# Performance work log

Measured on AMD Instinct MI355X. Metric: run time of the kernel, lower is better.

Reference implementation:

```python
import jax, jax.numpy as jnp
import numpy as np

NUM_CLASSES = 64  # matches labels fill_max
EMB_SCALE = 0.1   # keeps pairwise distances small so exp() stays finite (same regime as trained embeddings)


def setup_inputs() -> dict:
    key = jax.random.key(0)
    k1, k2 = jax.random.split(key)
    embeddings = jax.random.normal(k1, (8192, 128), dtype=jnp.float32) * EMB_SCALE
    labels = jax.random.randint(k2, (8192,), 0, NUM_CLASSES, dtype=jnp.int64 if jax.config.jax_enable_x64 else jnp.int32)
    return {"embeddings": embeddings, "labels": labels}


def reference(embeddings, labels):
    # Squared-euclidean distance matrix: ||xi||^2 + ||xj||^2 - 2 xi.xj   [N,N]
    sq = jnp.sum(embeddings * embeddings, axis=1)
    D = sq[:, None] + sq[None, :] - 2.0 * (embeddings @ embeddings.T)

    N = embeddings.shape[0]
    same = labels[:, None] == labels[None, :]          # [N,N] same-label mask
    neg = jnp.logical_not(same)

    # Z_i = sum over negatives n of exp(D[i,n]); then for pair (i,j):
    # sum_n exp(D[i,n] - D[i,j]) = Z_i * exp(-D[i,j])  (exact same math, factored)
    Z = jnp.sum(jnp.where(neg, jnp.exp(D), 0.0), axis=1)  # [N]

    # anchor-positive pairs: combinations(label_indices, 2) => i<j, same label
    iu = jnp.arange(N)
    pair_mask = same & (iu[:, None] < iu[None, :])

    # per-pair loss: log(1 + sum_n exp(D[a,n] - D[a,p]))
    L = jnp.log1p(Z[:, None] * jnp.exp(-D))            # [N,N]

    row_sum = jnp.sum(jnp.where(pair_mask, L, 0.0), axis=1)   # anchor i contributes pairs with label labels[i]
    row_cnt = jnp.sum(pair_mask, axis=1).astype(L.dtype)

    label_sum = jax.ops.segment_sum(row_sum, labels, num_segments=NUM_CLASSES)
    label_cnt = jax.ops.segment_sum(row_cnt, labels, num_segments=NUM_CLASSES)

    valid = label_cnt > 0                               # classes with >=2 members
    label_mean = jnp.where(valid, label_sum / jnp.maximum(label_cnt, 1.0), 0.0)
    n_valid = jnp.sum(valid)
    loss = jnp.sum(label_mean) / jnp.maximum(n_valid, 1).astype(L.dtype)
    return loss
```

## Files before the change

### kernel.cpp

```cpp
#include <hip/hip_runtime.h>
#include <hip/hip_bf16.h>
#include <math.h>

#define KD 128
#define NCLS 64
#define LOG2E 1.4426950408889634f
#define NEG2L -2.8853900817779268f
#define POS2L 2.8853900817779268f
#define LN2 0.6931471805599453f

typedef __attribute__((ext_vector_type(8))) short short8;
typedef __attribute__((ext_vector_type(4))) float f32x4;

__device__ inline void gload_lds16(const void* g, void* l) {
    __builtin_amdgcn_global_load_lds((const __attribute__((address_space(1))) unsigned int*)g,
                                     (__attribute__((address_space(3))) unsigned int*)l,
                                     16, 0, 0);
}
__device__ __forceinline__ float vexp2(float x) { float r; asm("v_exp_f32 %0, %1" : "=v"(r) : "v"(x)); return r; }
__device__ __forceinline__ float vlog2(float x) { float r; asm("v_log_f32 %0, %1" : "=v"(r) : "v"(x)); return r; }

__global__ __launch_bounds__(256) void prep_kernel(const float* __restrict__ emb,
                                                   const int* __restrict__ lab,
                                                   short* __restrict__ embb,
                                                   float* __restrict__ s2,
                                                   float* __restrict__ Z,
                                                   float* __restrict__ lsum,
                                                   int* __restrict__ cnt,
                                                   int* __restrict__ off,
                                                   int* __restrict__ list,
                                                   int* __restrict__ ctr, int N) {
    const int tid = threadIdx.x;
    if (blockIdx.x == gridDim.x - 1) {
        __shared__ int cntL[NCLS], offL[NCLS], curL[NCLS];
        if (tid < NCLS) cntL[tid] = 0;
        __syncthreads();
        for (int i = tid; i < N; i += 256) atomicAdd(&cntL[lab[i]], 1);
        __syncthreads();
        if (tid < NCLS) {
            int v = cntL[tid];
            int s = v;
            for (int m = 1; m < 64; m <<= 1) {
                int t2 = __shfl_up(s, m, 64);
                if (tid >= m) s += t2;
            }
            offL[tid] = s - v;
            curL[tid] = 0;
            off[tid] = s - v;
            cnt[tid] = v;
            lsum[tid] = 0.f;
        }
        if (tid == 0) ctr[0] = 0;
        __syncthreads();
        for (int i = tid; i < N; i += 256) {
            int c = lab[i];
            int p = atomicAdd(&curL[c], 1);
            list[offL[c] + p] = i;
        }
    } else {
        const int b = blockIdx.x;
        const int r0 = b * 16;
        const size_t base = (size_t)r0 * KD;
        float4 a = *(const float4*)&emb[base + (size_t)tid * 8];
        float4 bb = *(const float4*)&emb[base + (size_t)tid * 8 + 4];
        short8 o;
        __hip_bfloat16 h;
        h = __float2bfloat16(a.x);  o[0] = *(short*)&h;
        h = __float2bfloat16(a.y);  o[1] = *(short*)&h;
        h = __float2bfloat16(a.z);  o[2] = *(short*)&h;
        h = __float2bfloat16(a.w);  o[3] = *(short*)&h;
        h = __float2bfloat16(bb.x); o[4] = *(short*)&h;
        h = __float2bfloat16(bb.y); o[5] = *(short*)&h;
        h = __float2bfloat16(bb.z); o[6] = *(short*)&h;
        h = __float2bfloat16(bb.w); o[7] = *(short*)&h;
        *(short8*)&embb[base + (size_t)tid * 8] = o;
        float s = a.x * a.x + a.y * a.y + a.z * a.z + a.w * a.w
                + bb.x * bb.x + bb.y * bb.y + bb.z * bb.z + bb.w * bb.w;
        s += __shfl_xor(s, 1, 64);
        s += __shfl_xor(s, 2, 64);
        s += __shfl_xor(s, 4, 64);
        s += __shfl_xor(s, 8, 64);
        if ((tid & 15) == 0) s2[r0 + (tid >> 4)] = s * LOG2E;
        if (tid < 16) Z[r0 + tid] = 0.f;
    }
}

__global__ __launch_bounds__(256, 2) void zmain_kernel(const short* __restrict__ embb,
                                                       const float* __restrict__ s2,
                                                       float* __restrict__ Z, int N) {
    __shared__ short8 As8[128 * 16];
    __shared__ short8 Bs8[128 * 16];

    const int tid = threadIdx.x;
    const int w = tid >> 6, l = tid & 63;
    const int wr = w >> 1, wc = w & 1;
    const int g = blockIdx.x, it = blockIdx.y;
    const int i0 = it * 128;
    const short8* embv = (const short8*)embb;
    const int nd = 4 + ((g == 7 && it < 32) ? 1 : 0);

#pragma unroll
    for (int itr = 0; itr < 8; ++itr) {
        int lr = w * 32 + itr * 4 + (l >> 4);
        int c = (l & 15) ^ (lr & 7);
        gload_lds16(embv + (size_t)(i0 + lr) * 16 + c, &As8[w * 512 + itr * 64]);
    }
    {
        int j0 = ((it + g * 4) & 63) * 128;
#pragma unroll
        for (int itr = 0; itr < 8; ++itr) {
            int lr = w * 32 + itr * 4 + (l >> 4);
            int c = (l & 15) ^ (lr & 7);
            gload_lds16(embv + (size_t)(j0 + lr) * 16 + c, &Bs8[w * 512 + itr * 64]);
        }
    }

    float s2i[4][4];
#pragma unroll
    for (int mi = 0; mi < 4; ++mi)
#pragma unroll
        for (int r = 0; r < 4; ++r)
            s2i[mi][r] = s2[i0 + wr * 64 + mi * 16 + (l >> 4) * 4 + r];
    float zsum[4][4];
#pragma unroll
    for (int mi = 0; mi < 4; ++mi)
#pragma unroll
        for (int r = 0; r < 4; ++r) zsum[mi][r] = 0.f;

    __syncthreads();

    short8 af[4][4];
#pragma unroll
    for (int mi = 0; mi < 4; ++mi) {
        int row = wr * 64 + mi * 16 + (l & 15);
        int rs = row * 16, rx = row & 7;
#pragma unroll
        for (int ks = 0; ks < 4; ++ks) {
            int kc = ks * 4 + (l >> 4);
            af[mi][ks] = As8[rs + (kc ^ rx)];
        }
    }
    __syncthreads();

    for (int t = 0; t < nd; ++t) {
        const int d = (t < 4) ? (g * 4 + t) : 32;
        const int j0 = ((it + d) & 63) * 128;
        short8* rb = (t & 1) ? As8 : Bs8;
        short8* sb = (t & 1) ? Bs8 : As8;
        if (t + 1 < nd) {
            const int d1 = (t + 1 < 4) ? (g * 4 + t + 1) : 32;
            int j1 = ((it + d1) & 63) * 128;
#pragma unroll
            for (int itr = 0; itr < 8; ++itr) {
                int lr = w * 32 + itr * 4 + (l >> 4);
                int c = (l & 15) ^ (lr & 7);
                gload_lds16(embv + (size_t)(j1 + lr) * 16 + c, &sb[w * 512 + itr * 64]);
            }
        }

        f32x4 acc[4][4];
#pragma unroll
        for (int mi = 0; mi < 4; ++mi)
#pragma unroll
            for (int ni = 0; ni < 4; ++ni) acc[mi][ni] = (f32x4){0.f, 0.f, 0.f, 0.f};

#pragma unroll
        for (int ks = 0; ks < 4; ++ks) {
            short8 bf[4];
            int kc = ks * 4 + (l >> 4);
#pragma unroll
            for (int ni = 0; ni < 4; ++ni) {
                int row = wc * 64 + ni * 16 + (l & 15);
                bf[ni] = rb[row * 16 + (kc ^ (row & 7))];
            }
#pragma unroll
            for (int mi = 0; mi < 4; ++mi)
#pragma unroll
                for (int ni = 0; ni < 4; ++ni)
                    acc[mi][ni] = __builtin_amdgcn_mfma_f32_16x16x32_bf16(af[mi][ks], bf[ni], acc[mi][ni], 0, 0, 0);
        }

        float s2j[4];
#pragma unroll
        for (int ni = 0; ni < 4; ++ni)
            s2j[ni] = s2[j0 + wc * 64 + ni * 16 + (l & 15)];
        float cs[4] = {0.f, 0.f, 0.f, 0.f};
#pragma unroll
        for (int mi = 0; mi < 4; ++mi)
#pragma unroll
            for (int ni = 0; ni < 4; ++ni)
#pragma unroll
                for (int r = 0; r < 4; ++r) {
                    float e = vexp2(fmaf(NEG2L, acc[mi][ni][r], s2i[mi][r] + s2j[ni]));
                    zsum[mi][r] += e;
                    cs[ni] += e;
                }
        if (d > 0) {
#pragma unroll
            for (int ni = 0; ni < 4; ++ni) {
                float v = cs[ni];
                v += __shfl_xor(v, 16, 64);
                v += __shfl_xor(v, 32, 64);
                if ((l >> 4) == 0)
                    atomicAdd(&Z[j0 + wc * 64 + ni * 16 + (l & 15)], v);
            }
        }
        __syncthreads();
    }

#pragma unroll
    for (int mi = 0; mi < 4; ++mi)
#pragma unroll
        for (int r = 0; r < 4; ++r) {
            float v = zsum[mi][r];
            v += __shfl_xor(v, 1, 64);
            v += __shfl_xor(v, 2, 64);
            v += __shfl_xor(v, 4, 64);
            v += __shfl_xor(v, 8, 64);
            if ((l & 15) == 0)
                atomicAdd(&Z[i0 + wr * 64 + mi * 16 + (l >> 4) * 4 + r], v);
        }
}

__device__ __forceinline__ void gram_quad(const short8* Ms8, int l, int wr, int wc,
                                          int qi, int qj, f32x4 acc[4][4]) {
#pragma unroll
    for (int mi = 0; mi < 4; ++mi)
#pragma unroll
        for (int ni = 0; ni < 4; ++ni) acc[mi][ni] = (f32x4){0.f, 0.f, 0.f, 0.f};
#pragma unroll
    for (int ks = 0; ks < 4; ++ks) {
        short8 af[4], bf[4];
        int kc = ks * 4 + (l >> 4);
#pragma unroll
        for (int mi = 0; mi < 4; ++mi) {
            int row = qi * 128 + wr * 64 + mi * 16 + (l & 15);
            af[mi] = Ms8[row * 16 + (kc ^ (row & 7))];
        }
#pragma unroll
        for (int ni = 0; ni < 4; ++ni) {
            int row = qj * 128 + wc * 64 + ni * 16 + (l & 15);
            bf[ni] = Ms8[row * 16 + (kc ^ (row & 7))];
        }
#pragma unroll
        for (int mi = 0; mi < 4; ++mi)
#pragma unroll
            for (int ni = 0; ni < 4; ++ni)
                acc[mi][ni] = __builtin_amdgcn_mfma_f32_16x16x32_bf16(af[mi], bf[ni], acc[mi][ni], 0, 0, 0);
    }
}

__global__ __launch_bounds__(256, 2) void loss_kernel(const short* __restrict__ embb,
                                                      const float* __restrict__ s2,
                                                      const float* __restrict__ Z,
                                                      const int* __restrict__ cnt,
                                                      const int* __restrict__ off,
                                                      const int* __restrict__ list,
                                                      float* __restrict__ lsum,
                                                      int* __restrict__ ctr,
                                                      float* __restrict__ out) {
    __shared__ short8 Ms8[256 * 16];
    __shared__ float s2L[256], zfL[256], zsubL[256];
    __shared__ int gidL[256];
    __shared__ float red[4];
    __shared__ int lastB;

    const int h = blockIdx.x, c = blockIdx.y;
    const int k = cnt[c], base = off[c];
    const int kp = min(k, 256);
    const int tid = threadIdx.x;
    const int w = tid >> 6, l = tid & 63;
    const int wr = w >> 1, wc = w & 1;
    const short8* embv = (const short8*)embb;

    const bool active = (k >= 2) && !(h == 1 && kp <= 128);
    if (active) {
        {
            int gg = list[base + min(tid, k - 1)];
            bool ok = tid < k;
            s2L[tid] = ok ? s2[gg] : 0.f;
            gidL[tid] = ok ? gg : 0x7fffffff;
            zsubL[tid] = 0.f;
        }
#pragma unroll
        for (int itr = 0; itr < 16; ++itr) {
            int grp = w * 16 + itr;
            if (grp * 4 >= kp) break;
            int lr = grp * 4 + (l >> 4);
            int ch = (l & 15) ^ (lr & 7);
            int gg = list[base + min(lr, k - 1)];
            gload_lds16(embv + (size_t)gg * 16 + ch, &Ms8[grp * 64]);
        }
        __syncthreads();

        const int two = (kp > 128);
        f32x4 acc[4][4];

        for (int qq = 0; qq <= 2 * two; ++qq) {
            int qi = (qq == 2) ? 1 : 0;
            int qj = (qq == 0) ? 0 : 1;
            gram_quad(Ms8, l, wr, wc, qi, qj, acc);
            float rowsum[4][4];
#pragma unroll
            for (int mi = 0; mi < 4; ++mi)
#pragma unroll
                for (int r = 0; r < 4; ++r) rowsum[mi][r] = 0.f;
            float colsum[4] = {0.f, 0.f, 0.f, 0.f};
#pragma unroll
            for (int mi = 0; mi < 4; ++mi)
#pragma unroll
                for (int ni = 0; ni < 4; ++ni) {
                    int pB = qi * 128 + wr * 64 + mi * 16 + (l >> 4) * 4;
                    int qL = qj * 128 + wc * 64 + ni * 16 + (l & 15);
                    float sj = s2L[qL];
#pragma unroll
                    for (int r = 0; r < 4; ++r) {
                        float e = vexp2(fmaf(NEG2L, acc[mi][ni][r], s2L[pB + r] + sj));
                        e = ((pB + r) < k && qL < k) ? e : 0.f;
                        rowsum[mi][r] += e;
                        colsum[ni] += e;
                    }
                }
#pragma unroll
            for (int mi = 0; mi < 4; ++mi)
#pragma unroll
                for (int r = 0; r < 4; ++r) {
                    float v = rowsum[mi][r];
                    v += __shfl_xor(v, 1, 64);
                    v += __shfl_xor(v, 2, 64);
                    v += __shfl_xor(v, 4, 64);
                    v += __shfl_xor(v, 8, 64);
                    if ((l & 15) == 0)
                        atomicAdd(&zsubL[qi * 128 + wr * 64 + mi * 16 + (l >> 4) * 4 + r], v);
                }
            if (qi != qj) {
#pragma unroll
                for (int ni = 0; ni < 4; ++ni) {
                    float v = colsum[ni];
                    v += __shfl_xor(v, 16, 64);
                    v += __shfl_xor(v, 32, 64);
                    if ((l >> 4) == 0)
                        atomicAdd(&zsubL[qj * 128 + wc * 64 + ni * 16 + (l & 15)], v);
                }
            }
        }
        __syncthreads();
        zfL[tid] = (tid < k) ? (Z[gidL[tid]] - zsubL[tid]) : 0.f;
        __syncthreads();

        float part = 0.f;
        int q0 = (h == 0) ? 0 : 2;
        int q1 = (h == 0) ? (two ? 1 : 0) : 2;
        for (int qq = q0; qq <= q1; ++qq) {
            int qi = (qq == 2) ? 1 : 0;
            int qj = (qq == 0) ? 0 : 1;
            gram_quad(Ms8, l, wr, wc, qi, qj, acc);
#pragma unroll
            for (int mi = 0; mi < 4; ++mi)
#pragma unroll
                for (int ni = 0; ni < 4; ++ni) {
                    int qL = qj * 128 + wc * 64 + ni * 16 + (l & 15);
                    float sj = s2L[qL];
                    float zq = zfL[qL];
                    int gb = gidL[qL];
#pragma unroll
                    for (int r = 0; r < 4; ++r) {
                        int pL = qi * 128 + wr * 64 + mi * 16 + (l >> 4) * 4 + r;
                        bool valid = (pL < qL) && (qL < k);
                        float arg = fmaf(POS2L, acc[mi][ni][r], -(s2L[pL] + sj));
                        arg = valid ? arg : -160.f;
                        float e = vexp2(arg);
                        float z = (gidL[pL] < gb) ? zfL[pL] : zq;
                        part += vlog2(fmaf(z, e, 1.0f));
                    }
                }
        }

        for (int m = 32; m; m >>= 1) part += __shfl_xor(part, m, 64);
        if (l == 0) red[w] = part;
        __syncthreads();
        if (tid == 0)
            atomicAdd(&lsum[c], red[0] + red[1] + red[2] + red[3]);
    }

    __threadfence();
    if (tid == 0) lastB = (atomicAdd(ctr, 1) == 2 * NCLS - 1);
    __syncthreads();
    if (lastB) {
        __threadfence();
        if (tid < 64) {
            int cc = tid;
            float ls = atomicAdd(&lsum[cc], 0.0f);
            int kk = atomicAdd((int*)&cnt[cc], 0);
            float mean = 0.f;
            int valid = 0;
            long np = (long)kk * (kk - 1) / 2;
            if (np > 0) { mean = ls * LN2 / (float)np; valid = 1; }
            for (int m = 32; m; m >>= 1) {
                mean += __shfl_xor(mean, m, 64);
                valid += __shfl_xor(valid, m, 64);
            }
            if (cc == 0) out[0] = mean / (float)max(valid, 1);
        }
    }
}

extern "C" void kernel_launch(void* const* d_in, const int* in_sizes, int n_in,
                              void* d_out, int out_size, void* d_ws, size_t ws_size,
                              hipStream_t stream) {
    const float* emb = (const float*)d_in[0];
    const int* lab = (const int*)d_in[1];
    float* out = (float*)d_out;
    const int N = in_sizes[1];

    float* ws = (float*)d_ws;
    float* Z = ws;
    float* lsum = ws + N;
    int* cnt = (int*)(ws + N + NCLS);
    int* off = cnt + NCLS;
    int* ctr = off + NCLS;
    int* list = ctr + NCLS;
    float* s2 = (float*)(list + N);
    short* embb = (short*)(s2 + N);

    prep_kernel<<<N / 16 + 1, 256, 0, stream>>>(emb, lab, embb, s2, Z, lsum, cnt, off, list, ctr, N);
    dim3 zgrid(8, N / 128);
    zmain_kernel<<<zgrid, 256, 0, stream>>>(embb, s2, Z, N);
    dim3 lgrid(2, NCLS);
    loss_kernel<<<lgrid, 256, 0, stream>>>(embb, s2, Z, cnt, off, list, lsum, ctr, out);
}
```

Measured before the change: 122.5 us.

## Fuse prep, Z and loss stages into one cooperative kernel with grid syncs

```diff
diff --git a/kernel.cpp b/kernel.cpp
--- a/kernel.cpp
+++ b/kernel.cpp
@@ -1,6 +1,9 @@
 #include <hip/hip_runtime.h>
 #include <hip/hip_bf16.h>
+#include <hip/hip_cooperative_groups.h>
 #include <math.h>
+
+namespace cg = cooperative_groups;
 
 #define KD 128
 #define NCLS 64
@@ -12,6 +15,10 @@
 typedef __attribute__((ext_vector_type(8))) short short8;
 typedef __attribute__((ext_vector_type(4))) float f32x4;
 
+struct SMZ { short8 A[2048]; short8 B[2048]; };
+struct SML { short8 M[4096]; float s2L[256]; float zfL[256]; int gidL[256]; float red[4]; };
+struct SMS { int cnt[NCLS]; int off[NCLS]; int cur[NCLS]; };
+
 __device__ inline void gload_lds16(const void* g, void* l) {
     __builtin_amdgcn_global_load_lds((const __attribute__((address_space(1))) unsigned int*)g,
                                      (__attribute__((address_space(3))) unsigned int*)l,
@@ -19,6 +26,399 @@
 }
 __device__ __forceinline__ float vexp2(float x) { float r; asm("v_exp_f32 %0, %1" : "=v"(r) : "v"(x)); return r; }
 __device__ __forceinline__ float vlog2(float x) { float r; asm("v_log_f32 %0, %1" : "=v"(r) : "v"(x)); return r; }
+
+__device__ __forceinline__ void dev_cvt(int b, int tid, const float* __restrict__ emb,
+                                        short* __restrict__ embb, float* __restrict__ s2,
+                                        float* __restrict__ Z) {
+    const int r0 = b * 16;
+    const size_t base = (size_t)r0 * KD;
+    float4 a = *(const float4*)&emb[base + (size_t)tid * 8];
+    float4 bb = *(const float4*)&emb[base + (size_t)tid * 8 + 4];
+    short8 o;
+    __hip_bfloat16 h;
+    h = __float2bfloat16(a.x);  o[0] = *(short*)&h;
+    h = __float2bfloat16(a.y);  o[1] = *(short*)&h;
+    h = __float2bfloat16(a.z);  o[2] = *(short*)&h;
+    h = __float2bfloat16(a.w);  o[3] = *(short*)&h;
+    h = __float2bfloat16(bb.x); o[4] = *(short*)&h;
+    h = __float2bfloat16(bb.y); o[5] = *(short*)&h;
+    h = __float2bfloat16(bb.z); o[6] = *(short*)&h;
+    h = __float2bfloat16(bb.w); o[7] = *(short*)&h;
+    *(short8*)&embb[base + (size_t)tid * 8] = o;
+    float s = a.x * a.x + a.y * a.y + a.z * a.z + a.w * a.w
+            + bb.x * bb.x + bb.y * bb.y + bb.z * bb.z + bb.w * bb.w;
+    s += __shfl_xor(s, 1, 64);
+    s += __shfl_xor(s, 2, 64);
+    s += __shfl_xor(s, 4, 64);
+    s += __shfl_xor(s, 8, 64);
+    if ((tid & 15) == 0) s2[r0 + (tid >> 4)] = s * LOG2E;
+    if (tid < 16) Z[r0 + tid] = 0.f;
+}
+
+__device__ __forceinline__ void dev_scan(int tid, const int* __restrict__ lab,
+                                         int* __restrict__ cntG, int* __restrict__ offG,
+                                         int* __restrict__ list, float* __restrict__ lsum,
+                                         int* __restrict__ ctr, SMS* s, int N) {
+    if (tid < NCLS) { s->cnt[tid] = 0; lsum[tid] = 0.f; }
+    if (tid == 0) ctr[0] = 0;
+    __syncthreads();
+    for (int i = tid; i < N; i += 256) atomicAdd(&s->cnt[lab[i]], 1);
+    __syncthreads();
+    if (tid < NCLS) {
+        int v = s->cnt[tid];
+        int sc = v;
+        for (int m = 1; m < 64; m <<= 1) {
+            int t2 = __shfl_up(sc, m, 64);
+            if (tid >= m) sc += t2;
+        }
+        s->off[tid] = sc - v;
+        s->cur[tid] = 0;
+        offG[tid] = sc - v;
+        cntG[tid] = v;
+    }
+    __syncthreads();
+    for (int i = tid; i < N; i += 256) {
+        int c = lab[i];
+        int p = atomicAdd(&s->cur[c], 1);
+        list[s->off[c] + p] = i;
+    }
+}
+
+__device__ void dev_zmain(int g, int it, int tid, const short* __restrict__ embb,
+                          const float* __restrict__ s2, float* __restrict__ Z,
+                          short8* A8, short8* B8) {
+    const int w = tid >> 6, l = tid & 63;
+    const int wr = w >> 1, wc = w & 1;
+    const int i0 = it * 128;
+    const short8* embv = (const short8*)embb;
+    const int nd = 4 + ((g == 7 && it < 32) ? 1 : 0);
+
+#pragma unroll
+    for (int itr = 0; itr < 8; ++itr) {
+        int lr = w * 32 + itr * 4 + (l >> 4);
+        int c = (l & 15) ^ (lr & 7);
+        gload_lds16(embv + (size_t)(i0 + lr) * 16 + c, &A8[w * 512 + itr * 64]);
+    }
+    {
+        int j0 = ((it + g * 4) & 63) * 128;
+#pragma unroll
+        for (int itr = 0; itr < 8; ++itr) {
+            int lr = w * 32 + itr * 4 + (l >> 4);
+            int c = (l & 15) ^ (lr & 7);
+            gload_lds16(embv + (size_t)(j0 + lr) * 16 + c, &B8[w * 512 + itr * 64]);
+        }
+    }
+
+    float s2i[4][4];
+#pragma unroll
+    for (int mi = 0; mi < 4; ++mi)
+#pragma unroll
+        for (int r = 0; r < 4; ++r)
+            s2i[mi][r] = s2[i0 + wr * 64 + mi * 16 + (l >> 4) * 4 + r];
+    float zsum[4][4];
+#pragma unroll
+    for (int mi = 0; mi < 4; ++mi)
+#pragma unroll
+        for (int r = 0; r < 4; ++r) zsum[mi][r] = 0.f;
+
+    __syncthreads();
+
+    short8 af[4][4];
+#pragma unroll
+    for (int mi = 0; mi < 4; ++mi) {
+        int row = wr * 64 + mi * 16 + (l & 15);
+        int rs = row * 16, rx = row & 7;
+#pragma unroll
+        for (int ks = 0; ks < 4; ++ks) {
+            int kc = ks * 4 + (l >> 4);
+            af[mi][ks] = A8[rs + (kc ^ rx)];
+        }
+    }
+    __syncthreads();
+
+    for (int t = 0; t < nd; ++t) {
+        const int d = (t < 4) ? (g * 4 + t) : 32;
+        const int j0 = ((it + d) & 63) * 128;
+        short8* rb = (t & 1) ? A8 : B8;
+        short8* sb = (t & 1) ? B8 : A8;
+        if (t + 1 < nd) {
+            const int d1 = (t + 1 < 4) ? (g * 4 + t + 1) : 32;
+            int j1 = ((it + d1) & 63) * 128;
+#pragma unroll
+            for (int itr = 0; itr < 8; ++itr) {
+                int lr = w * 32 + itr * 4 + (l >> 4);
+                int c = (l & 15) ^ (lr & 7);
+                gload_lds16(embv + (size_t)(j1 + lr) * 16 + c, &sb[w * 512 + itr * 64]);
+            }
+        }
+
+        f32x4 acc[4][4];
+#pragma unroll
+        for (int mi = 0; mi < 4; ++mi)
+#pragma unroll
+            for (int ni = 0; ni < 4; ++ni) acc[mi][ni] = (f32x4){0.f, 0.f, 0.f, 0.f};
+
+#pragma unroll
+        for (int ks = 0; ks < 4; ++ks) {
+            short8 bf[4];
+            int kc = ks * 4 + (l >> 4);
+#pragma unroll
+            for (int ni = 0; ni < 4; ++ni) {
+                int row = wc * 64 + ni * 16 + (l & 15);
+                bf[ni] = rb[row * 16 + (kc ^ (row & 7))];
+            }
+#pragma unroll
+            for (int mi = 0; mi < 4; ++mi)
+#pragma unroll
+                for (int ni = 0; ni < 4; ++ni)
+                    acc[mi][ni] = __builtin_amdgcn_mfma_f32_16x16x32_bf16(af[mi][ks], bf[ni], acc[mi][ni], 0, 0, 0);
+        }
+
+        float s2j[4];
+#pragma unroll
+        for (int ni = 0; ni < 4; ++ni)
+            s2j[ni] = s2[j0 + wc * 64 + ni * 16 + (l & 15)];
+        float cs[4] = {0.f, 0.f, 0.f, 0.f};
+#pragma unroll
+        for (int mi = 0; mi < 4; ++mi)
+#pragma unroll
+            for (int ni = 0; ni < 4; ++ni)
+#pragma unroll
+                for (int r = 0; r < 4; ++r) {
+                    float e = vexp2(fmaf(NEG2L, acc[mi][ni][r], s2i[mi][r] + s2j[ni]));
+                    zsum[mi][r] += e;
+                    cs[ni] += e;
+                }
+        if (d > 0) {
+#pragma unroll
+            for (int ni = 0; ni < 4; ++ni) {
+                float v = cs[ni];
+                v += __shfl_xor(v, 16, 64);
+                v += __shfl_xor(v, 32, 64);
+                if ((l >> 4) == 0)
+                    atomicAdd(&Z[j0 + wc * 64 + ni * 16 + (l & 15)], v);
+            }
+        }
+        __syncthreads();
+    }
+
+#pragma unroll
+    for (int mi = 0; mi < 4; ++mi)
+#pragma unroll
+        for (int r = 0; r < 4; ++r) {
+            float v = zsum[mi][r];
+            v += __shfl_xor(v, 1, 64);
+            v += __shfl_xor(v, 2, 64);
+            v += __shfl_xor(v, 4, 64);
+            v += __shfl_xor(v, 8, 64);
+            if ((l & 15) == 0)
+                atomicAdd(&Z[i0 + wr * 64 + mi * 16 + (l >> 4) * 4 + r], v);
+        }
+}
+
+__device__ __forceinline__ void gram_quad(const short8* M8, int l, int wr, int wc,
+                                          int qi, int qj, f32x4 acc[4][4]) {
+#pragma unroll
+    for (int mi = 0; mi < 4; ++mi)
+#pragma unroll
+        for (int ni = 0; ni < 4; ++ni) acc[mi][ni] = (f32x4){0.f, 0.f, 0.f, 0.f};
+#pragma unroll
+    for (int ks = 0; ks < 4; ++ks) {
+        short8 af[4], bf[4];
+        int kc = ks * 4 + (l >> 4);
+#pragma unroll
+        for (int mi = 0; mi < 4; ++mi) {
+            int row = qi * 128 + wr * 64 + mi * 16 + (l & 15);
+            af[mi] = M8[row * 16 + (kc ^ (row & 7))];
+        }
+#pragma unroll
+        for (int ni = 0; ni < 4; ++ni) {
+            int row = qj * 128 + wc * 64 + ni * 16 + (l & 15);
+            bf[ni] = M8[row * 16 + (kc ^ (row & 7))];
+        }
+#pragma unroll
+        for (int mi = 0; mi < 4; ++mi)
+#pragma unroll
+            for (int ni = 0; ni < 4; ++ni)
+                acc[mi][ni] = __builtin_amdgcn_mfma_f32_16x16x32_bf16(af[mi], bf[ni], acc[mi][ni], 0, 0, 0);
+    }
+}
+
+__device__ void dev_loss(int h, int c, int tid, const short* __restrict__ embb,
+                         const float* __restrict__ s2, const float* __restrict__ Z,
+                         const int* __restrict__ cnt, const int* __restrict__ off,
+                         const int* __restrict__ list, float* __restrict__ lsum,
+                         SML* sm) {
+    const int k = cnt[c], base = off[c];
+    const int kp = min(k, 256);
+    const int w = tid >> 6, l = tid & 63;
+    const int wr = w >> 1, wc = w & 1;
+    const short8* embv = (const short8*)embb;
+
+    const bool active = (k >= 2) && !(h == 1 && kp <= 128);
+    if (!active) return;
+
+    {
+        int gg = list[base + min(tid, k - 1)];
+        bool ok = tid < k;
+        sm->s2L[tid] = ok ? s2[gg] : 0.f;
+        sm->gidL[tid] = ok ? gg : 0x7fffffff;
+        sm->zfL[tid] = 0.f;
+    }
+#pragma unroll
+    for (int itr = 0; itr < 16; ++itr) {
+        int grp = w * 16 + itr;
+        if (grp * 4 >= kp) break;
+        int lr = grp * 4 + (l >> 4);
+        int ch = (l & 15) ^ (lr & 7);
+        int gg = list[base + min(lr, k - 1)];
+        gload_lds16(embv + (size_t)gg * 16 + ch, &sm->M[grp * 64]);
+    }
+    __syncthreads();
+
+    const int two = (kp > 128);
+    f32x4 acc[4][4];
+
+    for (int qq = 0; qq <= 2 * two; ++qq) {
+        int qi = (qq == 2) ? 1 : 0;
+        int qj = (qq == 0) ? 0 : 1;
+        gram_quad(sm->M, l, wr, wc, qi, qj, acc);
+        float rowsum[4][4];
+#pragma unroll
+        for (int mi = 0; mi < 4; ++mi)
+#pragma unroll
+            for (int r = 0; r < 4; ++r) rowsum[mi][r] = 0.f;
+        float colsum[4] = {0.f, 0.f, 0.f, 0.f};
+#pragma unroll
+        for (int mi = 0; mi < 4; ++mi)
+#pragma unroll
+            for (int ni = 0; ni < 4; ++ni) {
+                int pB = qi * 128 + wr * 64 + mi * 16 + (l >> 4) * 4;
+                int qL = qj * 128 + wc * 64 + ni * 16 + (l & 15);
+                float sj = sm->s2L[qL];
+#pragma unroll
+                for (int r = 0; r < 4; ++r) {
+                    float e = vexp2(fmaf(NEG2L, acc[mi][ni][r], sm->s2L[pB + r] + sj));
+                    e = ((pB + r) < k && qL < k) ? e : 0.f;
+                    rowsum[mi][r] += e;
+                    colsum[ni] += e;
+                }
+            }
+#pragma unroll
+        for (int mi = 0; mi < 4; ++mi)
+#pragma unroll
+            for (int r = 0; r < 4; ++r) {
+                float v = rowsum[mi][r];
+                v += __shfl_xor(v, 1, 64);
+                v += __shfl_xor(v, 2, 64);
+                v += __shfl_xor(v, 4, 64);
+                v += __shfl_xor(v, 8, 64);
+                if ((l & 15) == 0)
+                    atomicAdd(&sm->zfL[qi * 128 + wr * 64 + mi * 16 + (l >> 4) * 4 + r], v);
+            }
+        if (qi != qj) {
+#pragma unroll
+            for (int ni = 0; ni < 4; ++ni) {
+                float v = colsum[ni];
+                v += __shfl_xor(v, 16, 64);
+                v += __shfl_xor(v, 32, 64);
+                if ((l >> 4) == 0)
+                    atomicAdd(&sm->zfL[qj * 128 + wc * 64 + ni * 16 + (l & 15)], v);
+            }
+        }
+    }
+    __syncthreads();
+    sm->zfL[tid] = (tid < k) ? (Z[sm->gidL[tid]] - sm->zfL[tid]) : 0.f;
+    __syncthreads();
+
+    float part = 0.f;
+    int q0 = (h == 0) ? 0 : 2;
+    int q1 = (h == 0) ? (two ? 1 : 0) : 2;
+    for (int qq = q0; qq <= q1; ++qq) {
+        int qi = (qq == 2) ? 1 : 0;
+        int qj = (qq == 0) ? 0 : 1;
+        gram_quad(sm->M, l, wr, wc, qi, qj, acc);
+#pragma unroll
+        for (int mi = 0; mi < 4; ++mi)
+#pragma unroll
+            for (int ni = 0; ni < 4; ++ni) {
+                int qL = qj * 128 + wc * 64 + ni * 16 + (l & 15);
+                float sj = sm->s2L[qL];
+                float zq = sm->zfL[qL];
+                int gb = sm->gidL[qL];
+#pragma unroll
+                for (int r = 0; r < 4; ++r) {
+                    int pL = qi * 128 + wr * 64 + mi * 16 + (l >> 4) * 4 + r;
+                    bool valid = (pL < qL) && (qL < k);
+                    float arg = fmaf(POS2L, acc[mi][ni][r], -(sm->s2L[pL] + sj));
+                    arg = valid ? arg : -160.f;
+                    float e = vexp2(arg);
+                    float z = (sm->gidL[pL] < gb) ? sm->zfL[pL] : zq;
+                    part += vlog2(fmaf(z, e, 1.0f));
+                }
+            }
+    }
+
+    for (int m = 32; m; m >>= 1) part += __shfl_xor(part, m, 64);
+    if (l == 0) sm->red[w] = part;
+    __syncthreads();
+    if (tid == 0)
+        atomicAdd(&lsum[c], sm->red[0] + sm->red[1] + sm->red[2] + sm->red[3]);
+}
+
+__device__ __forceinline__ void dev_tail(int tid, float* __restrict__ lsum,
+                                         int* __restrict__ cnt, int* __restrict__ ctr,
+                                         float* __restrict__ out, int* lastB) {
+    __threadfence();
+    if (tid == 0) *lastB = (atomicAdd(ctr, 1) == 2 * NCLS - 1);
+    __syncthreads();
+    if (*lastB) {
+        __threadfence();
+        if (tid < 64) {
+            int cc = tid;
+            float ls = atomicAdd(&lsum[cc], 0.0f);
+            int kk = atomicAdd(&cnt[cc], 0);
+            float mean = 0.f;
+            int valid = 0;
+            long np = (long)kk * (kk - 1) / 2;
+            if (np > 0) { mean = ls * LN2 / (float)np; valid = 1; }
+            for (int m = 32; m; m >>= 1) {
+                mean += __shfl_xor(mean, m, 64);
+                valid += __shfl_xor(valid, m, 64);
+            }
+            if (cc == 0) out[0] = mean / (float)max(valid, 1);
+        }
+    }
+}
+
+__global__ __launch_bounds__(256, 2) void fused_kernel(const float* __restrict__ emb,
+                                                       const int* __restrict__ lab,
+                                                       short* __restrict__ embb,
+                                                       float* __restrict__ s2,
+                                                       float* __restrict__ Z,
+                                                       float* __restrict__ lsum,
+                                                       int* __restrict__ cnt,
+                                                       int* __restrict__ off,
+                                                       int* __restrict__ list,
+                                                       int* __restrict__ ctr,
+                                                       float* __restrict__ out, int N) {
+    __shared__ union { SMZ z; SML l; SMS s; } sm;
+    __shared__ int lastB;
+    const int tid = threadIdx.x;
+    const int b = blockIdx.x;
+
+    dev_cvt(b, tid, emb, embb, s2, Z);
+    if (b == 0) dev_scan(tid, lab, cnt, off, list, lsum, ctr, &sm.s, N);
+    cg::this_grid().sync();
+
+    dev_zmain(b & 7, b >> 3, tid, embb, s2, Z, sm.z.A, sm.z.B);
+    cg::this_grid().sync();
+
+    if (b < 2 * NCLS) {
+        dev_loss(b & 1, b >> 1, tid, embb, s2, Z, cnt, off, list, lsum, &sm.l);
+        dev_tail(tid, lsum, cnt, ctr, out, &lastB);
+    }
+}
 
 __global__ __launch_bounds__(256) void prep_kernel(const float* __restrict__ emb,
                                                    const int* __restrict__ lab,
@@ -30,379 +430,33 @@
                                                    int* __restrict__ off,
                                                    int* __restrict__ list,
                                                    int* __restrict__ ctr, int N) {
-    const int tid = threadIdx.x;
-    if (blockIdx.x == gridDim.x - 1) {
-        __shared__ int cntL[NCLS], offL[NCLS], curL[NCLS];
-        if (tid < NCLS) cntL[tid] = 0;
-        __syncthreads();
-        for (int i = tid; i < N; i += 256) atomicAdd(&cntL[lab[i]], 1);
-        __syncthreads();
-        if (tid < NCLS) {
-            int v = cntL[tid];
-            int s = v;
-            for (int m = 1; m < 64; m <<= 1) {
-                int t2 = __shfl_up(s, m, 64);
-                if (tid >= m) s += t2;
-            }
-            offL[tid] = s - v;
-            curL[tid] = 0;
-            off[tid] = s - v;
-            cnt[tid] = v;
-            lsum[tid] = 0.f;
-        }
-        if (tid == 0) ctr[0] = 0;
-        __syncthreads();
-        for (int i = tid; i < N; i += 256) {
-            int c = lab[i];
-            int p = atomicAdd(&curL[c], 1);
-            list[offL[c] + p] = i;
-        }
-    } else {
-        const int b = blockIdx.x;
-        const int r0 = b * 16;
-        const size_t base = (size_t)r0 * KD;
-        float4 a = *(const float4*)&emb[base + (size_t)tid * 8];
-        float4 bb = *(const float4*)&emb[base + (size_t)tid * 8 + 4];
-        short8 o;
-        __hip_bfloat16 h;
-        h = __float2bfloat16(a.x);  o[0] = *(short*)&h;
-        h = __float2bfloat16(a.y);  o[1] = *(short*)&h;
-        h = __float2bfloat16(a.z);  o[2] = *(short*)&h;
-        h = __float2bfloat16(a.w);  o[3] = *(short*)&h;
-        h = __float2bfloat16(bb.x); o[4] = *(short*)&h;
-        h = __float2bfloat16(bb.y); o[5] = *(short*)&h;
-        h = __float2bfloat16(bb.z); o[6] = *(short*)&h;
-        h = __float2bfloat16(bb.w); o[7] = *(short*)&h;
-        *(short8*)&embb[base + (size_t)tid * 8] = o;
-        float s = a.x * a.x + a.y * a.y + a.z * a.z + a.w * a.w
-                + bb.x * bb.x + bb.y * bb.y + bb.z * bb.z + bb.w * bb.w;
-        s += __shfl_xor(s, 1, 64);
-        s += __shfl_xor(s, 2, 64);
-        s += __shfl_xor(s, 4, 64);
-        s += __shfl_xor(s, 8, 64);
-        if ((tid & 15) == 0) s2[r0 + (tid >> 4)] = s * LOG2E;
-        if (tid < 16) Z[r0 + tid] = 0.f;
-    }
+    __shared__ SMS s;
+    if (blockIdx.x == gridDim.x - 1)
+        dev_scan(threadIdx.x, lab, cnt, off, list, lsum, ctr, &s, N);
+    else
+        dev_cvt(blockIdx.x, threadIdx.x, emb, embb, s2, Z);
 }
 
 __global__ __launch_bounds__(256, 2) void zmain_kernel(const short* __restrict__ embb,
                                                        const float* __restrict__ s2,
                                                        float* __restrict__ Z, int N) {
-    __shared__ short8 As8[128 * 16];
-    __shared__ short8 Bs8[128 * 16];
-
-    const int tid = threadIdx.x;
-    const int w = tid >> 6, l = tid & 63;
-    const int wr = w >> 1, wc = w & 1;
-    const int g = blockIdx.x, it = blockIdx.y;
-    const int i0 = it * 128;
-    const short8* embv = (const short8*)embb;
-    const int nd = 4 + ((g == 7 && it < 32) ? 1 : 0);
-
-#pragma unroll
-    for (int itr = 0; itr < 8; ++itr) {
-        int lr = w * 32 + itr * 4 + (l >> 4);
-        int c = (l & 15) ^ (lr & 7);
-        gload_lds16(embv + (size_t)(i0 + lr) * 16 + c, &As8[w * 512 + itr * 64]);
-    }
-    {
-        int j0 = ((it + g * 4) & 63) * 128;
-#pragma unroll
-        for (int itr = 0; itr < 8; ++itr) {
-            int lr = w * 32 + itr * 4 + (l >> 4);
-            int c = (l & 15) ^ (lr & 7);
-            gload_lds16(embv + (size_t)(j0 + lr) * 16 + c, &Bs8[w * 512 + itr * 64]);
-        }
-    }
-
-    float s2i[4][4];
-#pragma unroll
-    for (int mi = 0; mi < 4; ++mi)
-#pragma unroll
-        for (int r = 0; r < 4; ++r)
-            s2i[mi][r] = s2[i0 + wr * 64 + mi * 16 + (l >> 4) * 4 + r];
-    float zsum[4][4];
-#pragma unroll
-    for (int mi = 0; mi < 4; ++mi)
-#pragma unroll
-        for (int r = 0; r < 4; ++r) zsum[mi][r] = 0.f;
-
-    __syncthreads();
-
-    short8 af[4][4];
-#pragma unroll
-    for (int mi = 0; mi < 4; ++mi) {
-        int row = wr * 64 + mi * 16 + (l & 15);
-        int rs = row * 16, rx = row & 7;
-#pragma unroll
-        for (int ks = 0; ks < 4; ++ks) {
-            int kc = ks * 4 + (l >> 4);
-            af[mi][ks] = As8[rs + (kc ^ rx)];
-        }
-    }
-    __syncthreads();
-
-    for (int t = 0; t < nd; ++t) {
-        const int d = (t < 4) ? (g * 4 + t) : 32;
-        const int j0 = ((it + d) & 63) * 128;
-        short8* rb = (t & 1) ? As8 : Bs8;
-        short8* sb = (t & 1) ? Bs8 : As8;
-        if (t + 1 < nd) {
-            const int d1 = (t + 1 < 4) ? (g * 4 + t + 1) : 32;
-            int j1 = ((it + d1) & 63) * 128;
-#pragma unroll
-            for (int itr = 0; itr < 8; ++itr) {
-                int lr = w * 32 + itr * 4 + (l >> 4);
-                int c = (l & 15) ^ (lr & 7);
-                gload_lds16(embv + (size_t)(j1 + lr) * 16 + c, &sb[w * 512 + itr * 64]);
-            }
-        }
-
-        f32x4 acc[4][4];
-#pragma unroll
-        for (int mi = 0; mi < 4; ++mi)
-#pragma unroll
-            for (int ni = 0; ni < 4; ++ni) acc[mi][ni] = (f32x4){0.f, 0.f, 0.f, 0.f};
-
-#pragma unroll
-        for (int ks = 0; ks < 4; ++ks) {
-            short8 bf[4];
-            int kc = ks * 4 + (l >> 4);
-#pragma unroll
-            for (int ni = 0; ni < 4; ++ni) {
-                int row = wc * 64 + ni * 16 + (l & 15);
-                bf[ni] = rb[row * 16 + (kc ^ (row & 7))];
-            }
-#pragma unroll
-            for (int mi = 0; mi < 4; ++mi)
-#pragma unroll
-                for (int ni = 0; ni < 4; ++ni)
-                    acc[mi][ni] = __builtin_amdgcn_mfma_f32_16x16x32_bf16(af[mi][ks], bf[ni], acc[mi][ni], 0, 0, 0);
-        }
-
-        float s2j[4];
-#pragma unroll
-        for (int ni = 0; ni < 4; ++ni)
-            s2j[ni] = s2[j0 + wc * 64 + ni * 16 + (l & 15)];
-        float cs[4] = {0.f, 0.f, 0.f, 0.f};
-#pragma unroll
-        for (int mi = 0; mi < 4; ++mi)
-#pragma unroll
-            for (int ni = 0; ni < 4; ++ni)
-#pragma unroll
-                for (int r = 0; r < 4; ++r) {
-                    float e = vexp2(fmaf(NEG2L, acc[mi][ni][r], s2i[mi][r] + s2j[ni]));
-                    zsum[mi][r] += e;
-                    cs[ni] += e;
-                }
-        if (d > 0) {
-#pragma unroll
-            for (int ni = 0; ni < 4; ++ni) {
-                float v = cs[ni];
-                v += __shfl_xor(v, 16, 64);
-                v += __shfl_xor(v, 32, 64);
-                if ((l >> 4) == 0)
-                    atomicAdd(&Z[j0 + wc * 64 + ni * 16 + (l & 15)], v);
-            }
-        }
-        __syncthreads();
-    }
-
-#pragma unroll
-    for (int mi = 0; mi < 4; ++mi)
-#pragma unroll
-        for (int r = 0; r < 4; ++r) {
-            float v = zsum[mi][r];
-            v += __shfl_xor(v, 1, 64);
-            v += __shfl_xor(v, 2, 64);
-            v += __shfl_xor(v, 4, 64);
-            v += __shfl_xor(v, 8, 64);
-            if ((l & 15) == 0)
-                atomicAdd(&Z[i0 + wr * 64 + mi * 16 + (l >> 4) * 4 + r], v);
-        }
-}
-
-__device__ __forceinline__ void gram_quad(const short8* Ms8, int l, int wr, int wc,
-                                          int qi, int qj, f32x4 acc[4][4]) {
-#pragma unroll
-    for (int mi = 0; mi < 4; ++mi)
-#pragma unroll
-        for (int ni = 0; ni < 4; ++ni) acc[mi][ni] = (f32x4){0.f, 0.f, 0.f, 0.f};
-#pragma unroll
-    for (int ks = 0; ks < 4; ++ks) {
-        short8 af[4], bf[4];
-        int kc = ks * 4 + (l >> 4);
-#pragma unroll
-        for (int mi = 0; mi < 4; ++mi) {
-            int row = qi * 128 + wr * 64 + mi * 16 + (l & 15);
-            af[mi] = Ms8[row * 16 + (kc ^ (row & 7))];
-        }
-#pragma unroll
-        for (int ni = 0; ni < 4; ++ni) {
-            int row = qj * 128 + wc * 64 + ni * 16 + (l & 15);
-            bf[ni] = Ms8[row * 16 + (kc ^ (row & 7))];
-        }
-#pragma unroll
-        for (int mi = 0; mi < 4; ++mi)
-#pragma unroll
-            for (int ni = 0; ni < 4; ++ni)
-                acc[mi][ni] = __builtin_amdgcn_mfma_f32_16x16x32_bf16(af[mi], bf[ni], acc[mi][ni], 0, 0, 0);
-    }
+    __shared__ SMZ z;
+    dev_zmain(blockIdx.x, blockIdx.y, threadIdx.x, embb, s2, Z, z.A, z.B);
 }
 
 __global__ __launch_bounds__(256, 2) void loss_kernel(const short* __restrict__ embb,
                                                       const float* __restrict__ s2,
                                                       const float* __restrict__ Z,
-                                                      const int* __restrict__ cnt,
+                                                      int* __restrict__ cnt,
                                                       const int* __restrict__ off,
                                                       const int* __restrict__ list,
                                                       float* __restrict__ lsum,
                                                       int* __restrict__ ctr,
                                                       float* __restrict__ out) {
-    __shared__ short8 Ms8[256 * 16];
-    __shared__ float s2L[256], zfL[256], zsubL[256];
-    __shared__ int gidL[256];
-    __shared__ float red[4];
+    __shared__ SML sml;
     __shared__ int lastB;
-
-    const int h = blockIdx.x, c = blockIdx.y;
-    const int k = cnt[c], base = off[c];
-    const int kp = min(k, 256);
-    const int tid = threadIdx.x;
-    const int w = tid >> 6, l = tid & 63;
-    const int wr = w >> 1, wc = w & 1;
-    const short8* embv = (const short8*)embb;
-
-    const bool active = (k >= 2) && !(h == 1 && kp <= 128);
-    if (active) {
-        {
-            int gg = list[base + min(tid, k - 1)];
-            bool ok = tid < k;
-            s2L[tid] = ok ? s2[gg] : 0.f;
-            gidL[tid] = ok ? gg : 0x7fffffff;
-            zsubL[tid] = 0.f;
-        }
-#pragma unroll
-        for (int itr = 0; itr < 16; ++itr) {
-            int grp = w * 16 + itr;
-            if (grp * 4 >= kp) break;
-            int lr = grp * 4 + (l >> 4);
-            int ch = (l & 15) ^ (lr & 7);
-            int gg = list[base + min(lr, k - 1)];
-            gload_lds16(embv + (size_t)gg * 16 + ch, &Ms8[grp * 64]);
-        }
-        __syncthreads();
-
-        const int two = (kp > 128);
-        f32x4 acc[4][4];
-
-        for (int qq = 0; qq <= 2 * two; ++qq) {
-            int qi = (qq == 2) ? 1 : 0;
-            int qj = (qq == 0) ? 0 : 1;
-            gram_quad(Ms8, l, wr, wc, qi, qj, acc);
-            float rowsum[4][4];
-#pragma unroll
-            for (int mi = 0; mi < 4; ++mi)
-#pragma unroll
-                for (int r = 0; r < 4; ++r) rowsum[mi][r] = 0.f;
-            float colsum[4] = {0.f, 0.f, 0.f, 0.f};
-#pragma unroll
-            for (int mi = 0; mi < 4; ++mi)
-#pragma unroll
-                for (int ni = 0; ni < 4; ++ni) {
-                    int pB = qi * 128 + wr * 64 + mi * 16 + (l >> 4) * 4;
-                    int qL = qj * 128 + wc * 64 + ni * 16 + (l & 15);
-                    float sj = s2L[qL];
-#pragma unroll
-                    for (int r = 0; r < 4; ++r) {
-                        float e = vexp2(fmaf(NEG2L, acc[mi][ni][r], s2L[pB + r] + sj));
-                        e = ((pB + r) < k && qL < k) ? e : 0.f;
-                        rowsum[mi][r] += e;
-                        colsum[ni] += e;
-                    }
-                }
-#pragma unroll
-            for (int mi = 0; mi < 4; ++mi)
-#pragma unroll
-                for (int r = 0; r < 4; ++r) {
-                    float v = rowsum[mi][r];
-                    v += __shfl_xor(v, 1, 64);
-                    v += __shfl_xor(v, 2, 64);
-                    v += __shfl_xor(v, 4, 64);
-                    v += __shfl_xor(v, 8, 64);
-                    if ((l & 15) == 0)
-                        atomicAdd(&zsubL[qi * 128 + wr * 64 + mi * 16 + (l >> 4) * 4 + r], v);
-                }
-            if (qi != qj) {
-#pragma unroll
-                for (int ni = 0; ni < 4; ++ni) {
-                    float v = colsum[ni];
-                    v += __shfl_xor(v, 16, 64);
-                    v += __shfl_xor(v, 32, 64);
-                    if ((l >> 4) == 0)
-                        atomicAdd(&zsubL[qj * 128 + wc * 64 + ni * 16 + (l & 15)], v);
-                }
-            }
-        }
-        __syncthreads();
-        zfL[tid] = (tid < k) ? (Z[gidL[tid]] - zsubL[tid]) : 0.f;
-        __syncthreads();
-
-        float part = 0.f;
-        int q0 = (h == 0) ? 0 : 2;
-        int q1 = (h == 0) ? (two ? 1 : 0) : 2;
-        for (int qq = q0; qq <= q1; ++qq) {
-            int qi = (qq == 2) ? 1 : 0;
-            int qj = (qq == 0) ? 0 : 1;
-            gram_quad(Ms8, l, wr, wc, qi, qj, acc);
-#pragma unroll
-            for (int mi = 0; mi < 4; ++mi)
-#pragma unroll
-                for (int ni = 0; ni < 4; ++ni) {
-                    int qL = qj * 128 + wc * 64 + ni * 16 + (l & 15);
-                    float sj = s2L[qL];
-                    float zq = zfL[qL];
-                    int gb = gidL[qL];
-#pragma unroll
-                    for (int r = 0; r < 4; ++r) {
-                        int pL = qi * 128 + wr * 64 + mi * 16 + (l >> 4) * 4 + r;
-                        bool valid = (pL < qL) && (qL < k);
-                        float arg = fmaf(POS2L, acc[mi][ni][r], -(s2L[pL] + sj));
-                        arg = valid ? arg : -160.f;
-                        float e = vexp2(arg);
-                        float z = (gidL[pL] < gb) ? zfL[pL] : zq;
-                        part += vlog2(fmaf(z, e, 1.0f));
-                    }
-                }
-        }
-
-        for (int m = 32; m; m >>= 1) part += __shfl_xor(part, m, 64);
-        if (l == 0) red[w] = part;
-        __syncthreads();
-        if (tid == 0)
-            atomicAdd(&lsum[c], red[0] + red[1] + red[2] + red[3]);
-    }
-
-    __threadfence();
-    if (tid == 0) lastB = (atomicAdd(ctr, 1) == 2 * NCLS - 1);
-    __syncthreads();
-    if (lastB) {
-        __threadfence();
-        if (tid < 64) {
-            int cc = tid;
-            float ls = atomicAdd(&lsum[cc], 0.0f);
-            int kk = atomicAdd((int*)&cnt[cc], 0);
-            float mean = 0.f;
-            int valid = 0;
-            long np = (long)kk * (kk - 1) / 2;
-            if (np > 0) { mean = ls * LN2 / (float)np; valid = 1; }
-            for (int m = 32; m; m >>= 1) {
-                mean += __shfl_xor(mean, m, 64);
-                valid += __shfl_xor(valid, m, 64);
-            }
-            if (cc == 0) out[0] = mean / (float)max(valid, 1);
-        }
-    }
+    dev_loss(blockIdx.x, blockIdx.y, threadIdx.x, embb, s2, Z, cnt, off, list, lsum, &sml);
+    dev_tail(threadIdx.x, lsum, cnt, ctr, out, &lastB);
 }
 
 extern "C" void kernel_launch(void* const* d_in, const int* in_sizes, int n_in,
@@ -411,7 +465,7 @@
     const float* emb = (const float*)d_in[0];
     const int* lab = (const int*)d_in[1];
     float* out = (float*)d_out;
-    const int N = in_sizes[1];
+    int N = in_sizes[1];
 
     float* ws = (float*)d_ws;
     float* Z = ws;
@@ -423,9 +477,16 @@
     float* s2 = (float*)(list + N);
     short* embb = (short*)(s2 + N);
 
-    prep_kernel<<<N / 16 + 1, 256, 0, stream>>>(emb, lab, embb, s2, Z, lsum, cnt, off, list, ctr, N);
-    dim3 zgrid(8, N / 128);
-    zmain_kernel<<<zgrid, 256, 0, stream>>>(embb, s2, Z, N);
-    dim3 lgrid(2, NCLS);
-    loss_kernel<<<lgrid, 256, 0, stream>>>(embb, s2, Z, cnt, off, list, lsum, ctr, out);
-}
+    void* args[] = {(void*)&emb, (void*)&lab, (void*)&embb, (void*)&s2, (void*)&Z,
+                    (void*)&lsum, (void*)&cnt, (void*)&off, (void*)&list, (void*)&ctr,
+                    (void*)&out, (void*)&N};
+    hipError_t err = hipLaunchCooperativeKernel((const void*)fused_kernel,
+                                                dim3(512), dim3(256), args, 0, stream);
+    if (err != hipSuccess) {
+        prep_kernel<<<N / 16 + 1, 256, 0, stream>>>(emb, lab, embb, s2, Z, lsum, cnt, off, list, ctr, N);
+        dim3 zgrid(8, N / 128);
+        zmain_kernel<<<zgrid, 256, 0, stream>>>(embb, s2, Z, N);
+        dim3 lgrid(2, NCLS);
+        loss_kernel<<<lgrid, 256, 0, stream>>>(embb, s2, Z, cnt, off, list, lsum, ctr, out);
+    }
+}
```

New measurement: 272.0 us. 2.22x slower.
